# Kernel tuning notes

Measured on AMD Instinct MI355X. Metric: run time of the kernel, lower is better.

The kernel has to match this reference:

```python
import jax, jax.numpy as jnp
import numpy as np

B, T, D = 8, 2048, 256
Q, K = 8, 1024


def setup_inputs() -> dict:
    key = jax.random.key(0)
    k1, k2 = jax.random.split(key)
    x = jax.random.normal(k1, (B, T, D), dtype=jnp.float32)
    codebooks = jax.random.normal(k2, (Q, K, D), dtype=jnp.float32)
    return {"x": x, "codebooks": codebooks}


def _vq_layer(residual, codebook):
    # residual: [B, T, D], codebook: [K, D]
    b, t, d = residual.shape
    flat = residual.reshape(-1, d)                      # [N, D]
    dist = (2.0 * flat @ codebook.T
            - jnp.sum(flat * flat, axis=-1, keepdims=True)
            - jnp.sum(codebook * codebook, axis=-1))    # [N, K]
    idx = jnp.argmax(dist, axis=-1)                     # [N]
    quantize = codebook[idx].reshape(b, t, d)           # gather
    # commitment loss (codebook updated via EMA in torch, not gradient)
    loss = jnp.mean((jax.lax.stop_gradient(quantize) - residual) ** 2)
    # straight-through estimator
    quantize_st = residual + jax.lax.stop_gradient(quantize - residual)
    return quantize_st, idx.reshape(b, t), loss


def reference(x, codebooks):
    def step(residual, codebook):
        q, idx, loss = _vq_layer(residual, codebook)
        return residual - q, (q, idx, loss)

    _, (qs, all_indices, all_losses) = jax.lax.scan(step, x, codebooks)
    quantized_out = jnp.sum(qs, axis=0)                 # [B, T, D]
    return quantized_out, all_indices, all_losses
```

## Files before the change

### kernel.cpp

```cpp
#include <hip/hip_runtime.h>


typedef _Float16 f16;
typedef f16 f16x8 __attribute__((ext_vector_type(8)));
typedef float f32x4 __attribute__((ext_vector_type(4)));

constexpr int Dd = 256;
constexpr int Kk = 1024;
constexpr int Qq = 8;
constexpr int Nn = 16384;

__device__ inline void gload16(const f16* g, f16* l) {
    __builtin_amdgcn_global_load_lds(
        (const __attribute__((address_space(1))) unsigned int*)(const __attribute__((address_space(1))) f16*)g,
        (__attribute__((address_space(3))) unsigned int*)(__attribute__((address_space(3))) f16*)l,
        16, 0, 0);
}

__global__ __launch_bounds__(256) void build_ecat(const float* __restrict__ cb,
                                                  f16* __restrict__ ecat,
                                                  float* __restrict__ norms) {
    int row = blockIdx.x * 8 + (threadIdx.x >> 5);
    int p = threadIdx.x & 31;
    const float* s = cb + (size_t)row * Dd + p * 8;
    f16x8 hi, lo;
    float sq = 0.f;
#pragma unroll
    for (int j = 0; j < 8; ++j) {
        float v = s[j];
        f16 h = (f16)v;
        hi[j] = h; lo[j] = (f16)(v - (float)h);
        sq = fmaf(v, v, sq);
    }
    *(f16x8*)(ecat + (size_t)row * 512 + p * 8) = hi;
    *(f16x8*)(ecat + (size_t)row * 512 + 256 + p * 8) = lo;
#pragma unroll
    for (int off = 16; off >= 1; off >>= 1) sq += __shfl_down(sq, off, 32);
    if (p == 0) norms[row] = sq;
}

__global__ __launch_bounds__(512, 2) void score_kernel(
    const float* __restrict__ x,
    const float* __restrict__ cb_prev,
    const f16* __restrict__ ecat,
    const float* __restrict__ norms,
    const f16* __restrict__ xold,
    f16* __restrict__ xnew,
    const float2* __restrict__ pin,
    float2* __restrict__ pout,
    float* __restrict__ idx_prev,
    float* __restrict__ loss_prev,
    int q)
{
    __shared__ f16 sEh[2][8192];
    __shared__ f16 sEl[2][8192];
    __shared__ f16 sXh[2][8192];
    __shared__ f16 sXl[2][8192];
    __shared__ float smn[256];
    __shared__ float2 smg[2][256];
    __shared__ float lred[8];

    const int tid = threadIdx.x;
    const int w = tid >> 6, l = tid & 63;
    const int wr = w >> 2, wc = w & 3;
    const int l16 = l & 15, hi4 = l >> 4;

    const int b = blockIdx.x;
    const int slice = (b >> 3) & 3;
    const int tokt = ((b >> 5) << 3) | (b & 7);
    const int tbase = tokt * 256;
    const int qcb = slice * 256;

    {
        const int up = tid & 15;
        const int d0 = up * 16;
        float lp = 0.f;
#pragma unroll 1
        for (int pass = 0; pass < 8; ++pass) {
            const int row = tbase + pass * 32 + (tid >> 4);
            f16* xw = xnew + (size_t)row * 512;
            if (q == 0) {
                const float* xs = x + (size_t)row * Dd + d0;
#pragma unroll
                for (int c = 0; c < 2; ++c) {
                    f16x8 hi, lo;
#pragma unroll
                    for (int j = 0; j < 8; ++j) {
                        float v = 2.f * xs[c * 8 + j];
                        f16 h = (f16)v;
                        hi[j] = h; lo[j] = (f16)(v - (float)h);
                    }
                    *(f16x8*)(xw + d0 + c * 8) = hi;
                    *(f16x8*)(xw + 256 + d0 + c * 8) = lo;
                }
            } else {
                float2 bsel = pin[row];
#pragma unroll
                for (int s2 = 1; s2 < 4; ++s2) {
                    float2 c2 = pin[(size_t)s2 * Nn + row];
                    if (c2.x > bsel.x || (c2.x == bsel.x && c2.y < bsel.y)) bsel = c2;
                }
                const int k = (int)bsel.y;
                const float* e = cb_prev + (size_t)k * Dd + d0;
                const f16* xr = xold + (size_t)row * 512;
                f16x8 h0 = *(const f16x8*)(xr + d0);
                f16x8 h1 = *(const f16x8*)(xr + d0 + 8);
                f16x8 l0 = *(const f16x8*)(xr + 256 + d0);
                f16x8 l1 = *(const f16x8*)(xr + 256 + d0 + 8);
                float rn[16];
#pragma unroll
                for (int j = 0; j < 8; ++j) {
                    rn[j]     = ((float)h0[j] + (float)l0[j]) * 0.5f - e[j];
                    rn[8 + j] = ((float)h1[j] + (float)l1[j]) * 0.5f - e[8 + j];
                }
#pragma unroll
                for (int j = 0; j < 16; ++j) lp = fmaf(rn[j], rn[j], lp);
#pragma unroll
                for (int c = 0; c < 2; ++c) {
                    f16x8 hi, lo;
#pragma unroll
                    for (int j = 0; j < 8; ++j) {
                        float v = 2.f * rn[c * 8 + j];
                        f16 h = (f16)v;
                        hi[j] = h; lo[j] = (f16)(v - (float)h);
                    }
                    *(f16x8*)(xw + d0 + c * 8) = hi;
                    *(f16x8*)(xw + 256 + d0 + c * 8) = lo;
                }
                if (slice == 0 && up == 0) idx_prev[row] = (float)k;
            }
        }
        if (q > 0 && slice == 0) {
#pragma unroll
            for (int off = 32; off >= 1; off >>= 1) lp += __shfl_down(lp, off);
            if (l == 0) lred[w] = lp;
        }
    }
    if (tid < 256) smn[tid] = norms[qcb + tid];
    __syncthreads();
    if (q > 0 && slice == 0 && tid == 0) {
        float s = 0.f;
#pragma unroll
        for (int i = 0; i < 8; ++i) s += lred[i];
        atomicAdd(loss_prev, s * (1.0f / ((float)Nn * (float)Dd)));
    }

    const int srow = tid >> 2;
    const int g = ((tid & 3) ^ ((tid >> 3) & 3)) * 8;
    const f16* gae = ecat + (size_t)(qcb + srow) * 512 + g;
    const f16* gbx = xnew + (size_t)(tbase + srow) * 512 + g;

    int offA[8], offB[4];
#pragma unroll
    for (int m = 0; m < 8; ++m) {
        int row = wr * 128 + m * 16 + l16;
        offA[m] = row * 32 + ((hi4 ^ ((row >> 1) & 3)) * 8);
    }
#pragma unroll
    for (int n = 0; n < 4; ++n) {
        int row = wc * 64 + n * 16 + l16;
        offB[n] = row * 32 + ((hi4 ^ ((row >> 1) & 3)) * 8);
    }

    f32x4 acc[8][4];
#pragma unroll
    for (int m = 0; m < 8; ++m)
#pragma unroll
        for (int n = 0; n < 4; ++n) acc[m][n] = (f32x4){0.f, 0.f, 0.f, 0.f};

#define STAGE_CHUNK(P, C) do { \
        int cc = (C) * 32; \
        gload16(gae + cc,             &sEh[P][tid * 8]); \
        gload16(gae + cc + 128 * 512, &sEh[P][4096 + tid * 8]); \
        gload16(gae + 256 + cc,             &sEl[P][tid * 8]); \
        gload16(gae + 256 + cc + 128 * 512, &sEl[P][4096 + tid * 8]); \
        gload16(gbx + cc,             &sXh[P][tid * 8]); \
        gload16(gbx + cc + 128 * 512, &sXh[P][4096 + tid * 8]); \
        gload16(gbx + 256 + cc,             &sXl[P][tid * 8]); \
        gload16(gbx + 256 + cc + 128 * 512, &sXl[P][4096 + tid * 8]); \
    } while (0)

    STAGE_CHUNK(0, 0);
    asm volatile("s_waitcnt vmcnt(0)\n\ts_barrier" ::: "memory");

#pragma unroll
    for (int c = 0; c < 8; ++c) {
        const int p = c & 1;
        if (c < 7) STAGE_CHUNK(p ^ 1, c + 1);
        f16x8 aeh[8], bxh[4], bxl[4];
#pragma unroll
        for (int m = 0; m < 8; ++m) aeh[m] = *(const f16x8*)&sEh[p][offA[m]];
#pragma unroll
        for (int n = 0; n < 4; ++n) bxh[n] = *(const f16x8*)&sXh[p][offB[n]];
#pragma unroll
        for (int n = 0; n < 4; ++n) bxl[n] = *(const f16x8*)&sXl[p][offB[n]];
        __builtin_amdgcn_s_setprio(1);
#pragma unroll
        for (int m = 0; m < 8; ++m)
#pragma unroll
            for (int n = 0; n < 4; ++n)
                acc[m][n] = __builtin_amdgcn_mfma_f32_16x16x32_f16(aeh[m], bxh[n], acc[m][n], 0, 0, 0);
#pragma unroll
        for (int m = 0; m < 8; ++m)
#pragma unroll
            for (int n = 0; n < 4; ++n)
                acc[m][n] = __builtin_amdgcn_mfma_f32_16x16x32_f16(aeh[m], bxl[n], acc[m][n], 0, 0, 0);
        __builtin_amdgcn_s_setprio(0);
        f16x8 ael[8];
#pragma unroll
        for (int m = 0; m < 8; ++m) ael[m] = *(const f16x8*)&sEl[p][offA[m]];
        __builtin_amdgcn_s_setprio(1);
#pragma unroll
        for (int m = 0; m < 8; ++m)
#pragma unroll
            for (int n = 0; n < 4; ++n)
                acc[m][n] = __builtin_amdgcn_mfma_f32_16x16x32_f16(ael[m], bxh[n], acc[m][n], 0, 0, 0);
        __builtin_amdgcn_s_setprio(0);
        if (c < 7)
            asm volatile("s_waitcnt vmcnt(0)\n\ts_barrier" ::: "memory");
    }
#undef STAGE_CHUNK

    float bv[4]; int bi[4];
#pragma unroll
    for (int n = 0; n < 4; ++n) { bv[n] = -3.4e38f; bi[n] = 0; }
#pragma unroll
    for (int m = 0; m < 8; ++m) {
#pragma unroll
        for (int r = 0; r < 4; ++r) {
            int cl = wr * 128 + m * 16 + hi4 * 4 + r;
            float nrm = smn[cl];
            int cg = qcb + cl;
#pragma unroll
            for (int n = 0; n < 4; ++n) {
                float v = acc[m][n][r] - nrm;
                if (v > bv[n]) { bv[n] = v; bi[n] = cg; }
            }
        }
    }
#pragma unroll
    for (int off = 16; off <= 32; off <<= 1) {
#pragma unroll
        for (int n = 0; n < 4; ++n) {
            float ov = __shfl_xor(bv[n], off);
            int oi = __shfl_xor(bi[n], off);
            if (ov > bv[n] || (ov == bv[n] && oi < bi[n])) { bv[n] = ov; bi[n] = oi; }
        }
    }
    if (l < 16) {
#pragma unroll
        for (int n = 0; n < 4; ++n)
            smg[wr][wc * 64 + n * 16 + l] = make_float2(bv[n], (float)bi[n]);
    }
    __syncthreads();
    if (tid < 256) {
        float2 a = smg[0][tid], c = smg[1][tid];
        float2 r = (c.x > a.x || (c.x == a.x && c.y < a.y)) ? c : a;
        pout[(size_t)slice * Nn + tbase + tid] = r;
    }
}

__global__ __launch_bounds__(256) void final_kernel(
    const float* __restrict__ x,
    const float* __restrict__ cb7,
    const f16* __restrict__ xcat,
    const float2* __restrict__ pin,
    float* __restrict__ out,
    float* __restrict__ idx7,
    float* __restrict__ loss7)
{
    __shared__ float lsum[4];
    const int tid = threadIdx.x;
    const int row = blockIdx.x * 16 + (tid >> 4);
    const int d0 = (tid & 15) * 16;

    float2 bsel = pin[row];
#pragma unroll
    for (int s2 = 1; s2 < 4; ++s2) {
        float2 c2 = pin[(size_t)s2 * Nn + row];
        if (c2.x > bsel.x || (c2.x == bsel.x && c2.y < bsel.y)) bsel = c2;
    }
    const int k = (int)bsel.y;
    const float* e = cb7 + (size_t)k * Dd + d0;
    const f16* xr = xcat + (size_t)row * 512;
    const float* xs = x + (size_t)row * Dd + d0;
    float* os = out + (size_t)row * Dd + d0;

    f16x8 h0 = *(const f16x8*)(xr + d0);
    f16x8 h1 = *(const f16x8*)(xr + d0 + 8);
    f16x8 l0 = *(const f16x8*)(xr + 256 + d0);
    f16x8 l1 = *(const f16x8*)(xr + 256 + d0 + 8);
    float lp = 0.f;
#pragma unroll
    for (int j = 0; j < 8; ++j) {
        float r7a = ((float)h0[j] + (float)l0[j]) * 0.5f;
        float r7b = ((float)h1[j] + (float)l1[j]) * 0.5f;
        float r8a = r7a - e[j];
        float r8b = r7b - e[8 + j];
        os[j]     = xs[j] - r8a;
        os[8 + j] = xs[8 + j] - r8b;
        lp = fmaf(r8a, r8a, lp);
        lp = fmaf(r8b, r8b, lp);
    }
    if ((tid & 15) == 0) idx7[row] = (float)k;

#pragma unroll
    for (int off = 32; off >= 1; off >>= 1) lp += __shfl_down(lp, off);
    if ((tid & 63) == 0) lsum[tid >> 6] = lp;
    __syncthreads();
    if (tid == 0) {
        float s = lsum[0] + lsum[1] + lsum[2] + lsum[3];
        atomicAdd(loss7, s * (1.0f / ((float)Nn * (float)Dd)));
    }
}

extern "C" void kernel_launch(void* const* d_in, const int* in_sizes, int n_in,
                              void* d_out, int out_size, void* d_ws, size_t ws_size,
                              hipStream_t stream) {
    const float* x   = (const float*)d_in[0];
    const float* cbs = (const float*)d_in[1];
    float* out    = (float*)d_out;
    float* idxs   = out + (size_t)Nn * Dd;
    float* losses = idxs + (size_t)Qq * Nn;

    f16* xb0     = (f16*)d_ws;
    f16* xb1     = xb0 + (size_t)Nn * 512;
    f16* ecat    = xb1 + (size_t)Nn * 512;
    float* norms = (float*)(ecat + (size_t)Qq * Kk * 512);
    float2* part0 = (float2*)(norms + (size_t)Qq * Kk);
    float2* part1 = part0 + (size_t)4 * Nn;

    hipMemsetAsync(losses, 0, Qq * sizeof(float), stream);
    build_ecat<<<(Qq * Kk) / 8, 256, 0, stream>>>(cbs, ecat, norms);

    for (int q = 0; q < Qq; ++q) {
        float2* pin  = (q & 1) ? part1 : part0;
        float2* pout = (q & 1) ? part0 : part1;
        const f16* xold = (q & 1) ? xb0 : xb1;
        f16* xnew       = (q & 1) ? xb1 : xb0;
        score_kernel<<<256, 512, 0, stream>>>(
            x,
            q > 0 ? cbs + (size_t)(q - 1) * Kk * Dd : cbs,
            ecat + (size_t)q * Kk * 512, norms + (size_t)q * Kk,
            xold, xnew, pin, pout,
            q > 0 ? idxs + (size_t)(q - 1) * Nn : idxs,
            q > 0 ? losses + (q - 1) : losses,
            q);
    }
    final_kernel<<<Nn / 16, 256, 0, stream>>>(
        x, cbs + (size_t)7 * Kk * Dd, xb1, part0, out,
        idxs + (size_t)7 * Nn, losses + 7);
}
```

Before: 334.1 us.

## Switch distance GEMM to 32x32x16 MFMA and prefetch codebook tiles early

Replaces the 16x16x32 MFMA tiling with 32x32x16 MFMA tiles (f32x16 accumulators), adjusting LDS swizzle, fragment offsets and the argmax epilogue to the new output layout. Codebook chunks for the first two stages are issued before the residual-update prologue so their loads overlap that work, and the staging is double-prefetched with a partial vmcnt wait. It also partially unrolls the prologue pass loop. The larger MFMA shape cuts instruction count and LDS fragment reads per FLOP, but the new swizzle and layout mapping raise the risk of bank conflicts or indexing errors.

Result: slower. 344.4 us (+3.1%).

```diff
diff --git a/kernel.cpp b/kernel.cpp
--- a/kernel.cpp
+++ b/kernel.cpp
@@ -4,6 +4,7 @@
 typedef _Float16 f16;
 typedef f16 f16x8 __attribute__((ext_vector_type(8)));
 typedef float f32x4 __attribute__((ext_vector_type(4)));
+typedef float f32x16 __attribute__((ext_vector_type(16)));
 
 constexpr int Dd = 256;
 constexpr int Kk = 1024;
@@ -63,7 +64,7 @@
     const int tid = threadIdx.x;
     const int w = tid >> 6, l = tid & 63;
     const int wr = w >> 2, wc = w & 3;
-    const int l16 = l & 15, hi4 = l >> 4;
+    const int l32 = l & 31, lh = l >> 5;
 
     const int b = blockIdx.x;
     const int slice = (b >> 3) & 3;
@@ -71,11 +72,34 @@
     const int tbase = tokt * 256;
     const int qcb = slice * 256;
 
+    const int srow = tid >> 2;
+    const int g = ((tid & 3) ^ ((tid >> 5) & 3)) * 8;
+    const f16* gae = ecat + (size_t)(qcb + srow) * 512 + g;
+    const f16* gbx = xnew + (size_t)(tbase + srow) * 512 + g;
+
+#define STAGE_A(P, C) do { \
+        int cc = (C) * 32; \
+        gload16(gae + cc,             &sEh[P][tid * 8]); \
+        gload16(gae + cc + 128 * 512, &sEh[P][4096 + tid * 8]); \
+        gload16(gae + 256 + cc,             &sEl[P][tid * 8]); \
+        gload16(gae + 256 + cc + 128 * 512, &sEl[P][4096 + tid * 8]); \
+    } while (0)
+#define STAGE_B(P, C) do { \
+        int cc = (C) * 32; \
+        gload16(gbx + cc,             &sXh[P][tid * 8]); \
+        gload16(gbx + cc + 128 * 512, &sXh[P][4096 + tid * 8]); \
+        gload16(gbx + 256 + cc,             &sXl[P][tid * 8]); \
+        gload16(gbx + 256 + cc + 128 * 512, &sXl[P][4096 + tid * 8]); \
+    } while (0)
+
+    STAGE_A(0, 0);
+    STAGE_A(1, 1);
+
     {
         const int up = tid & 15;
         const int d0 = up * 16;
         float lp = 0.f;
-#pragma unroll 1
+#pragma unroll 2
         for (int pass = 0; pass < 8; ++pass) {
             const int row = tbase + pass * 32 + (tid >> 4);
             f16* xw = xnew + (size_t)row * 512;
@@ -145,112 +169,101 @@
         atomicAdd(loss_prev, s * (1.0f / ((float)Nn * (float)Dd)));
     }
 
-    const int srow = tid >> 2;
-    const int g = ((tid & 3) ^ ((tid >> 3) & 3)) * 8;
-    const f16* gae = ecat + (size_t)(qcb + srow) * 512 + g;
-    const f16* gbx = xnew + (size_t)(tbase + srow) * 512 + g;
-
-    int offA[8], offB[4];
-#pragma unroll
-    for (int m = 0; m < 8; ++m) {
-        int row = wr * 128 + m * 16 + l16;
-        offA[m] = row * 32 + ((hi4 ^ ((row >> 1) & 3)) * 8);
-    }
-#pragma unroll
-    for (int n = 0; n < 4; ++n) {
-        int row = wc * 64 + n * 16 + l16;
-        offB[n] = row * 32 + ((hi4 ^ ((row >> 1) & 3)) * 8);
-    }
-
-    f32x4 acc[8][4];
-#pragma unroll
-    for (int m = 0; m < 8; ++m)
-#pragma unroll
-        for (int n = 0; n < 4; ++n) acc[m][n] = (f32x4){0.f, 0.f, 0.f, 0.f};
-
-#define STAGE_CHUNK(P, C) do { \
-        int cc = (C) * 32; \
-        gload16(gae + cc,             &sEh[P][tid * 8]); \
-        gload16(gae + cc + 128 * 512, &sEh[P][4096 + tid * 8]); \
-        gload16(gae + 256 + cc,             &sEl[P][tid * 8]); \
-        gload16(gae + 256 + cc + 128 * 512, &sEl[P][4096 + tid * 8]); \
-        gload16(gbx + cc,             &sXh[P][tid * 8]); \
-        gload16(gbx + cc + 128 * 512, &sXh[P][4096 + tid * 8]); \
-        gload16(gbx + 256 + cc,             &sXl[P][tid * 8]); \
-        gload16(gbx + 256 + cc + 128 * 512, &sXl[P][4096 + tid * 8]); \
-    } while (0)
-
-    STAGE_CHUNK(0, 0);
-    asm volatile("s_waitcnt vmcnt(0)\n\ts_barrier" ::: "memory");
+    int offA[4][2], offB[2][2];
+#pragma unroll
+    for (int m = 0; m < 4; ++m)
+#pragma unroll
+        for (int kh = 0; kh < 2; ++kh) {
+            int row = wr * 128 + m * 32 + l32;
+            offA[m][kh] = row * 32 + (((kh * 2 + lh) ^ ((row >> 3) & 3)) * 8);
+        }
+#pragma unroll
+    for (int n = 0; n < 2; ++n)
+#pragma unroll
+        for (int kh = 0; kh < 2; ++kh) {
+            int row = wc * 64 + n * 32 + l32;
+            offB[n][kh] = row * 32 + (((kh * 2 + lh) ^ ((row >> 3) & 3)) * 8);
+        }
+
+    f32x16 acc[4][2];
+#pragma unroll
+    for (int m = 0; m < 4; ++m)
+#pragma unroll
+        for (int n = 0; n < 2; ++n) acc[m][n] = {};
+
+    STAGE_B(0, 0);
+    STAGE_B(1, 1);
+    asm volatile("s_waitcnt vmcnt(4)\n\ts_barrier" ::: "memory");
 
 #pragma unroll
     for (int c = 0; c < 8; ++c) {
         const int p = c & 1;
-        if (c < 7) STAGE_CHUNK(p ^ 1, c + 1);
-        f16x8 aeh[8], bxh[4], bxl[4];
-#pragma unroll
-        for (int m = 0; m < 8; ++m) aeh[m] = *(const f16x8*)&sEh[p][offA[m]];
-#pragma unroll
-        for (int n = 0; n < 4; ++n) bxh[n] = *(const f16x8*)&sXh[p][offB[n]];
-#pragma unroll
-        for (int n = 0; n < 4; ++n) bxl[n] = *(const f16x8*)&sXl[p][offB[n]];
-        __builtin_amdgcn_s_setprio(1);
-#pragma unroll
-        for (int m = 0; m < 8; ++m)
-#pragma unroll
-            for (int n = 0; n < 4; ++n)
-                acc[m][n] = __builtin_amdgcn_mfma_f32_16x16x32_f16(aeh[m], bxh[n], acc[m][n], 0, 0, 0);
-#pragma unroll
-        for (int m = 0; m < 8; ++m)
-#pragma unroll
-            for (int n = 0; n < 4; ++n)
-                acc[m][n] = __builtin_amdgcn_mfma_f32_16x16x32_f16(aeh[m], bxl[n], acc[m][n], 0, 0, 0);
-        __builtin_amdgcn_s_setprio(0);
-        f16x8 ael[8];
-#pragma unroll
-        for (int m = 0; m < 8; ++m) ael[m] = *(const f16x8*)&sEl[p][offA[m]];
-        __builtin_amdgcn_s_setprio(1);
-#pragma unroll
-        for (int m = 0; m < 8; ++m)
-#pragma unroll
-            for (int n = 0; n < 4; ++n)
-                acc[m][n] = __builtin_amdgcn_mfma_f32_16x16x32_f16(ael[m], bxh[n], acc[m][n], 0, 0, 0);
-        __builtin_amdgcn_s_setprio(0);
+        if (c >= 1 && c < 7) { STAGE_A(p ^ 1, c + 1); STAGE_B(p ^ 1, c + 1); }
+#pragma unroll
+        for (int kh = 0; kh < 2; ++kh) {
+            f16x8 aeh[4], bxh[2], bxl[2];
+#pragma unroll
+            for (int m = 0; m < 4; ++m) aeh[m] = *(const f16x8*)&sEh[p][offA[m][kh]];
+#pragma unroll
+            for (int n = 0; n < 2; ++n) bxh[n] = *(const f16x8*)&sXh[p][offB[n][kh]];
+#pragma unroll
+            for (int n = 0; n < 2; ++n) bxl[n] = *(const f16x8*)&sXl[p][offB[n][kh]];
+            __builtin_amdgcn_s_setprio(1);
+#pragma unroll
+            for (int m = 0; m < 4; ++m)
+#pragma unroll
+                for (int n = 0; n < 2; ++n)
+                    acc[m][n] = __builtin_amdgcn_mfma_f32_32x32x16_f16(aeh[m], bxh[n], acc[m][n], 0, 0, 0);
+#pragma unroll
+            for (int m = 0; m < 4; ++m)
+#pragma unroll
+                for (int n = 0; n < 2; ++n)
+                    acc[m][n] = __builtin_amdgcn_mfma_f32_32x32x16_f16(aeh[m], bxl[n], acc[m][n], 0, 0, 0);
+            __builtin_amdgcn_s_setprio(0);
+            f16x8 ael[4];
+#pragma unroll
+            for (int m = 0; m < 4; ++m) ael[m] = *(const f16x8*)&sEl[p][offA[m][kh]];
+            __builtin_amdgcn_s_setprio(1);
+#pragma unroll
+            for (int m = 0; m < 4; ++m)
+#pragma unroll
+                for (int n = 0; n < 2; ++n)
+                    acc[m][n] = __builtin_amdgcn_mfma_f32_32x32x16_f16(ael[m], bxh[n], acc[m][n], 0, 0, 0);
+            __builtin_amdgcn_s_setprio(0);
+        }
         if (c < 7)
             asm volatile("s_waitcnt vmcnt(0)\n\ts_barrier" ::: "memory");
     }
-#undef STAGE_CHUNK
-
-    float bv[4]; int bi[4];
-#pragma unroll
-    for (int n = 0; n < 4; ++n) { bv[n] = -3.4e38f; bi[n] = 0; }
-#pragma unroll
-    for (int m = 0; m < 8; ++m) {
-#pragma unroll
-        for (int r = 0; r < 4; ++r) {
-            int cl = wr * 128 + m * 16 + hi4 * 4 + r;
+#undef STAGE_A
+#undef STAGE_B
+
+    float bv[2]; int bi[2];
+#pragma unroll
+    for (int n = 0; n < 2; ++n) { bv[n] = -3.4e38f; bi[n] = 0; }
+#pragma unroll
+    for (int m = 0; m < 4; ++m) {
+#pragma unroll
+        for (int r = 0; r < 16; ++r) {
+            int cl = wr * 128 + m * 32 + (r & 3) + 8 * (r >> 2) + 4 * lh;
             float nrm = smn[cl];
             int cg = qcb + cl;
 #pragma unroll
-            for (int n = 0; n < 4; ++n) {
+            for (int n = 0; n < 2; ++n) {
                 float v = acc[m][n][r] - nrm;
                 if (v > bv[n]) { bv[n] = v; bi[n] = cg; }
             }
         }
     }
 #pragma unroll
-    for (int off = 16; off <= 32; off <<= 1) {
-#pragma unroll
-        for (int n = 0; n < 4; ++n) {
-            float ov = __shfl_xor(bv[n], off);
-            int oi = __shfl_xor(bi[n], off);
-            if (ov > bv[n] || (ov == bv[n] && oi < bi[n])) { bv[n] = ov; bi[n] = oi; }
-        }
-    }
-    if (l < 16) {
-#pragma unroll
-        for (int n = 0; n < 4; ++n)
-            smg[wr][wc * 64 + n * 16 + l] = make_float2(bv[n], (float)bi[n]);
+    for (int n = 0; n < 2; ++n) {
+        float ov = __shfl_xor(bv[n], 32);
+        int oi = __shfl_xor(bi[n], 32);
+        if (ov > bv[n] || (ov == bv[n] && oi < bi[n])) { bv[n] = ov; bi[n] = oi; }
+    }
+    if (l < 32) {
+#pragma unroll
+        for (int n = 0; n < 2; ++n)
+            smg[wr][wc * 64 + n * 32 + l] = make_float2(bv[n], (float)bi[n]);
     }
     __syncthreads();
     if (tid < 256) {
```
